# Performance work log

Measured on AMD Instinct MI355X. Metric: run time of the kernel, lower is better.

Reference implementation:

```python
import jax, jax.numpy as jnp
import numpy as np

EPS = 0.01
EXPD_WEIGHT = 1.0
COMP_WEIGHT = 1.0
NUM_CLASSES = 32
M, D = 262144, 128


def setup_inputs() -> dict:
    key = jax.random.key(0)
    k1, k2 = jax.random.split(key)
    cls_score = jax.random.normal(k1, (M, D), dtype=jnp.float32)
    label = jax.random.randint(k2, (M,), 0, NUM_CLASSES)
    return {"cls_score": cls_score, "label": label}


def _logdet(X):
    sgn, ld = jnp.linalg.slogdet(X)
    return sgn * ld


def reference(cls_score, label):
    m, d = cls_score.shape
    m_f = jnp.asarray(m, cls_score.dtype)
    # expansion term: logdet(c * Z^T Z) / 2, c = d / (m * eps)
    c = d / (m_f * EPS)
    cov = cls_score.T @ cls_score  # [d, d]
    loss_expd = _logdet(c * cov) / 2.0

    # compression term: sum_j m_j/(2m) * logdet(c_j * Z_j^T Z_j)
    def per_class(j):
        mask = (label == j).astype(cls_score.dtype)  # [m]
        m_j = mask.sum()
        safe_mj = jnp.maximum(m_j, 1.0)
        c_j = d / (safe_mj * EPS)
        # Z_j^T Z_j == (mask * Z)^T Z, honoring the boolean subset without gather
        cov_j = (cls_score * mask[:, None]).T @ cls_score  # [d, d]
        ld_j = _logdet(c_j * cov_j)
        return jnp.where(m_j > 0, ld_j * m_j / (2.0 * m_f), 0.0)

    comps = jax.lax.map(per_class, jnp.arange(NUM_CLASSES))  # [J]
    loss_comp = comps.sum()

    # MCR2Loss.forward with return_all=False
    return loss_comp * COMP_WEIGHT - loss_expd * EXPD_WEIGHT
```

## Files before the change

### kernel.cpp

```cpp
#include <hip/hip_runtime.h>
#include <math.h>

#define D 128
#define NCLS 32
#define TSLOT 16
#define CHUNK 256

typedef float f32x16 __attribute__((ext_vector_type(16)));
typedef short bf16x8 __attribute__((ext_vector_type(8)));

__global__ void zero_k(int* hist) {
  int t = threadIdx.x;
  if (t < NCLS) hist[t] = 0;
}

__global__ __launch_bounds__(64) void hist_blk_k(const int* __restrict__ label, int M,
                                                 int NB, int* __restrict__ blkhist_t,
                                                 int* __restrict__ hist) {
  __shared__ int h[NCLS];
  const int lane = threadIdx.x;
  const int b = blockIdx.x;
  if (lane < NCLS) h[lane] = 0;
  __syncthreads();
  const int s0 = b * CHUNK;
#pragma unroll
  for (int it = 0; it < CHUNK / 64; ++it) {
    int i = s0 + it * 64 + lane;
    if (i < M) atomicAdd(&h[label[i]], 1);
  }
  __syncthreads();
  if (lane < NCLS) {
    blkhist_t[lane * NB + b] = h[lane];
    atomicAdd(&hist[lane], h[lane]);
  }
}

__global__ void prefix_k(const int* __restrict__ hist, int* __restrict__ cstart) {
  if (threadIdx.x == 0) {
    int run = 0;
    for (int j = 0; j < NCLS; ++j) { cstart[j] = run; run += hist[j]; }
    cstart[NCLS] = run;
  }
}

__global__ __launch_bounds__(64) void base_k(const int* __restrict__ blkhist_t,
                                             const int* __restrict__ cstart, int NB,
                                             int* __restrict__ base_t) {
  const int j = blockIdx.x;
  const int lane = threadIdx.x;
  const int K = (NB + 63) / 64;
  int vals[32];
  int run = 0;
  for (int k = 0; k < K; ++k) {
    int b = lane * K + k;
    int v = (b < NB) ? blkhist_t[j * NB + b] : 0;
    vals[k] = v;
    run += v;
  }
  int incl = run;
  for (int off = 1; off < 64; off <<= 1) {
    int o = __shfl_up(incl, off);
    if (lane >= off) incl += o;
  }
  int pos = cstart[j] + (incl - run);
  for (int k = 0; k < K; ++k) {
    int b = lane * K + k;
    if (b < NB) base_t[j * NB + b] = pos;
    pos += vals[k];
  }
}

__global__ __launch_bounds__(64) void scatter2_k(const int* __restrict__ label, int M,
                                                 int NB, const int* __restrict__ base_t,
                                                 int* __restrict__ idxbuf) {
  __shared__ int cur[NCLS];
  const int b = blockIdx.x;
  const int lane = threadIdx.x;
  if (lane < NCLS) cur[lane] = base_t[lane * NB + b];
  __syncthreads();
  const int s0 = b * CHUNK;
#pragma unroll
  for (int it = 0; it < CHUNK / 64; ++it) {
    int i = s0 + it * 64 + lane;
    int j = (i < M) ? label[i] : -1;
    unsigned long long mask = 0;
#pragma unroll
    for (int q = 0; q < NCLS; ++q) {
      unsigned long long mm = __ballot(j == q);
      if (j == q) mask = mm;
    }
    if (j >= 0) {
      int myoff = __popcll(mask & ((1ull << lane) - 1ull));
      int basec = cur[j];
      idxbuf[basec + myoff] = i;
      if (myoff == 0) cur[j] = basec + __popcll(mask);
    }
    __syncthreads();
  }
}

__device__ inline void bsplit(float x, short& hi, short& lo) {
  unsigned u = __float_as_uint(x);
  unsigned rh = u + 0x7fffu + ((u >> 16) & 1u);
  unsigned short h = (unsigned short)(rh >> 16);
  float hf = __uint_as_float((unsigned)h << 16);
  float l = x - hf;
  unsigned ul = __float_as_uint(l);
  unsigned rl = ul + 0x7fffu + ((ul >> 16) & 1u);
  hi = (short)h;
  lo = (short)(rl >> 16);
}

__global__ __launch_bounds__(512, 4) void cov_k(const float* __restrict__ Z,
                                                const int* __restrict__ idxbuf,
                                                const int* __restrict__ hist,
                                                const int* __restrict__ cstart,
                                                float* __restrict__ partials) {
  __shared__ __attribute__((aligned(16))) char arena[66048];

  const int b = blockIdx.x;
  const int cls = b / TSLOT, slot = b % TSLOT;
  const int t = threadIdx.x;
  const int lane = t & 63;
  const int w = t >> 6;
  const int r = w & 3;
  const int pass = w >> 2;
  const int col4 = t & 31;
  const int rg = t >> 5;

  const int mj = hist[cls];
  const int seg0 = cstart[cls];
  const int segend = seg0 + mj;
  const int nch = (mj + 63) / 64;

  f32x16 acc[4];
#pragma unroll
  for (int c = 0; c < 4; ++c)
#pragma unroll
    for (int i = 0; i < 16; ++i) acc[c][i] = 0.f;

  const int pcol = r * 32 + (lane & 31);
  const int h = lane >> 5;
  const int aswz = (pcol & 7) << 4;
  char* const bbase = arena + (pass ? 16384 : 0);

  float4 pv[4];
  {
    const int ch = slot;
    const int r0 = seg0 + ch * 64;
#pragma unroll
    for (int i = 0; i < 4; ++i) {
      int gr = r0 + rg * 4 + i;
      if (ch < nch && gr < segend) {
        int ridx = idxbuf[gr];
        pv[i] = *(const float4*)(Z + (size_t)ridx * D + col4 * 4);
      } else {
        pv[i] = make_float4(0.f, 0.f, 0.f, 0.f);
      }
    }
  }

  for (int ch = slot; ch < nch; ch += TSLOT) {
    __syncthreads();
    {
      float xs[4][4];
      xs[0][0] = pv[0].x; xs[0][1] = pv[0].y; xs[0][2] = pv[0].z; xs[0][3] = pv[0].w;
      xs[1][0] = pv[1].x; xs[1][1] = pv[1].y; xs[1][2] = pv[1].z; xs[1][3] = pv[1].w;
      xs[2][0] = pv[2].x; xs[2][1] = pv[2].y; xs[2][2] = pv[2].z; xs[2][3] = pv[2].w;
      xs[3][0] = pv[3].x; xs[3][1] = pv[3].y; xs[3][2] = pv[3].z; xs[3][3] = pv[3].w;
#pragma unroll
      for (int j = 0; j < 4; ++j) {
        short h0, h1, h2, h3, l0, l1, l2, l3;
        bsplit(xs[0][j], h0, l0);
        bsplit(xs[1][j], h1, l1);
        bsplit(xs[2][j], h2, l2);
        bsplit(xs[3][j], h3, l3);
        const int cc = col4 * 4 + j;
        const int off = cc * 128 + ((rg * 8) ^ ((cc & 7) << 4));
        *(short4*)(arena + off) = make_short4(h0, h1, h2, h3);
        *(short4*)(arena + 16384 + off) = make_short4(l0, l1, l2, l3);
      }
    }
    __syncthreads();
    {
      const int chn = ch + TSLOT;
      const int r0 = seg0 + chn * 64;
#pragma unroll
      for (int i = 0; i < 4; ++i) {
        int gr = r0 + rg * 4 + i;
        if (chn < nch && gr < segend) {
          int ridx = idxbuf[gr];
          pv[i] = *(const float4*)(Z + (size_t)ridx * D + col4 * 4);
        } else {
          pv[i] = make_float4(0.f, 0.f, 0.f, 0.f);
        }
      }
    }
#pragma unroll
    for (int kk = 0; kk < 4; ++kk) {
      const int koff = kk * 32 + h * 16;
      bf16x8 a = *(const bf16x8*)(arena + pcol * 128 + (koff ^ aswz));
#pragma unroll
      for (int c = 0; c < 4; ++c) {
        const int qcol = c * 32 + (lane & 31);
        bf16x8 bb = *(const bf16x8*)(bbase + qcol * 128 + (koff ^ ((qcol & 7) << 4)));
        acc[c] = __builtin_amdgcn_mfma_f32_32x32x16_bf16(a, bb, acc[c], 0, 0, 0);
      }
    }
  }

  __syncthreads();
  float* g2 = (float*)arena;
  if (pass == 1) {
#pragma unroll
    for (int c = 0; c < 4; ++c)
#pragma unroll
      for (int i = 0; i < 16; ++i) {
        int prow = r * 32 + (i & 3) + 8 * (i >> 2) + 4 * h;
        int qcol = c * 32 + (lane & 31);
        g2[prow * 129 + qcol] = acc[c][i];
      }
  }
  __syncthreads();
  if (pass == 0) {
    size_t base = (size_t)b * (D * D);
#pragma unroll
    for (int c = 0; c < 4; ++c)
#pragma unroll
      for (int i = 0; i < 16; ++i) {
        int prow = r * 32 + (i & 3) + 8 * (i >> 2) + 4 * h;
        int qcol = c * 32 + (lane & 31);
        float v = acc[c][i] + g2[prow * 129 + qcol] + g2[qcol * 129 + prow];
        partials[base + (size_t)prow * D + qcol] = v;
      }
  }
}

__global__ void reduce_k(const float* __restrict__ partials, float* __restrict__ covs) {
  int e = blockIdx.x * blockDim.x + threadIdx.x;
  double tot = 0.0;
  for (int j = 0; j < NCLS; ++j) {
    double s = 0.0;
    for (int t = 0; t < TSLOT; ++t)
      s += (double)partials[(size_t)(j * TSLOT + t) * (D * D) + e];
    covs[(size_t)j * (D * D) + e] = (float)s;
    tot += s;
  }
  covs[(size_t)NCLS * (D * D) + e] = (float)tot;
}

template <int T>
__device__ void trailing_upd(float (*As)[132], int pbase, int tid) {
  const int ty = tid >> 4, tx = tid & 15;
  const int r0 = pbase + 32 + ty * T;
  const int c0 = pbase + 32 + tx * T;
  float acc[T][T];
#pragma unroll
  for (int a = 0; a < T; ++a)
#pragma unroll
    for (int b = 0; b < T; ++b) acc[a][b] = 0.f;
#pragma unroll
  for (int j0 = 0; j0 < 32; j0 += 8) {
    float ar[T][8];
#pragma unroll
    for (int a = 0; a < T; ++a) {
      float4 v0 = *(const float4*)&As[r0 + a][pbase + j0];
      float4 v1 = *(const float4*)&As[r0 + a][pbase + j0 + 4];
      ar[a][0] = v0.x; ar[a][1] = v0.y; ar[a][2] = v0.z; ar[a][3] = v0.w;
      ar[a][4] = v1.x; ar[a][5] = v1.y; ar[a][6] = v1.z; ar[a][7] = v1.w;
    }
#pragma unroll
    for (int b = 0; b < T; ++b) {
      float4 w0 = *(const float4*)&As[c0 + b][pbase + j0];
      float4 w1 = *(const float4*)&As[c0 + b][pbase + j0 + 4];
      float acb[8] = {w0.x, w0.y, w0.z, w0.w, w1.x, w1.y, w1.z, w1.w};
#pragma unroll
      for (int jj = 0; jj < 8; ++jj)
#pragma unroll
        for (int a = 0; a < T; ++a)
          acc[a][b] = fmaf(ar[a][jj], acb[jj], acc[a][b]);
    }
  }
#pragma unroll
  for (int a = 0; a < T; ++a)
#pragma unroll
    for (int b = 0; b < T; ++b)
      As[r0 + a][c0 + b] -= acc[a][b];
}

__global__ __launch_bounds__(256, 1) void chol_k(const float* __restrict__ covs,
                                                 const int* __restrict__ hist,
                                                 int Mtot, double* __restrict__ results) {
  __shared__ float As[128][132];
  __shared__ float PlT[32][36];
  __shared__ float invd[32];
  __shared__ float colbuf[32];
  __shared__ double red[64];
  const int j = blockIdx.x;
  const float* A = covs + (size_t)j * (D * D);
  const int tid = threadIdx.x;
  const int lane = tid & 63;
  const int w = tid >> 6;

#pragma unroll
  for (int it = 0; it < 16; ++it) {
    int e = it * 1024 + tid * 4;
    int r = e >> 7, c = e & 127;
    *(float4*)&As[r][c] = *(const float4*)&A[e];
  }
  __syncthreads();

  double lda = 0.0;
#pragma unroll 1
  for (int p = 0; p < 4; ++p) {
    const int pbase = p * 32;
    if (w == 0) {
      const int l = lane & 31;
      float row[32];
#pragma unroll
      for (int c4 = 0; c4 < 8; ++c4) {
        float4 v = *(const float4*)&As[pbase + l][pbase + c4 * 4];
        row[c4 * 4 + 0] = v.x; row[c4 * 4 + 1] = v.y;
        row[c4 * 4 + 2] = v.z; row[c4 * 4 + 3] = v.w;
      }
      float mypiv = 1.f, myinv = 0.f;
#pragma unroll
      for (int k = 0; k < 32; ++k) {
        colbuf[l] = row[k];
        float cb[32];
#pragma unroll
        for (int q = 0; q < 8; ++q) {
          float4 v = *(const float4*)&colbuf[q * 4];
          cb[q * 4 + 0] = v.x; cb[q * 4 + 1] = v.y;
          cb[q * 4 + 2] = v.z; cb[q * 4 + 3] = v.w;
        }
        float piv = cb[k];
        float inv = rsqrtf(piv);
        inv = inv * (1.5f - 0.5f * piv * inv * inv);
        if (lane == k) { mypiv = piv; myinv = inv; }
        float tmul = row[k] * (inv * inv);
#pragma unroll
        for (int c = k + 1; c < 32; ++c)
          row[c] = fmaf(-tmul, cb[c], row[c]);
        row[k] *= inv;
      }
      if (lane < 32) {
#pragma unroll
        for (int c = 0; c < 32; ++c) PlT[c][lane] = row[c];
        invd[lane] = myinv;
      }
      lda += log((double)mypiv);
    }
    __syncthreads();
    const int N2 = 96 - pbase;
    if (tid < N2) {
      const int R = pbase + 32 + tid;
      float s[32];
#pragma unroll
      for (int c4 = 0; c4 < 8; ++c4) {
        float4 v = *(const float4*)&As[R][pbase + c4 * 4];
        s[c4 * 4 + 0] = v.x; s[c4 * 4 + 1] = v.y;
        s[c4 * 4 + 2] = v.z; s[c4 * 4 + 3] = v.w;
      }
#pragma unroll
      for (int i = 0; i < 32; ++i) {
        float xi = s[i] * invd[i];
        s[i] = xi;
#pragma unroll
        for (int jj = i + 1; jj < 32; ++jj)
          s[jj] = fmaf(-xi, PlT[i][jj], s[jj]);
      }
#pragma unroll
      for (int c4 = 0; c4 < 8; ++c4)
        *(float4*)&As[R][pbase + c4 * 4] =
            make_float4(s[c4 * 4], s[c4 * 4 + 1], s[c4 * 4 + 2], s[c4 * 4 + 3]);
    }
    __syncthreads();
    if (N2 == 96) trailing_upd<6>(As, pbase, tid);
    else if (N2 == 64) trailing_upd<4>(As, pbase, tid);
    else if (N2 == 32) trailing_upd<2>(As, pbase, tid);
    __syncthreads();
  }

  if (w == 0) red[lane] = lda;
  __syncthreads();
  if (tid == 0) {
    double lsum = 0.0;
    for (int i = 0; i < 64; ++i) lsum += red[i];
    if (j < NCLS) {
      int mj = hist[j];
      double res = 0.0;
      if (mj > 0) {
        double cj = (double)D / ((double)mj * 0.01);
        res = ((double)D * log(cj) + lsum) * (double)mj / (2.0 * (double)Mtot);
      }
      results[j] = res;
    } else {
      double c = (double)D / ((double)Mtot * 0.01);
      results[NCLS] = ((double)D * log(c) + lsum) * 0.5;
    }
  }
}

__global__ void final_k(const double* __restrict__ results, float* __restrict__ out) {
  if (threadIdx.x == 0 && blockIdx.x == 0) {
    double s = 0.0;
    for (int j = 0; j < NCLS; ++j) s += results[j];
    out[0] = (float)(s - results[NCLS]);
  }
}

extern "C" void kernel_launch(void* const* d_in, const int* in_sizes, int n_in,
                              void* d_out, int out_size, void* d_ws, size_t ws_size,
                              hipStream_t stream) {
  const float* Z = (const float*)d_in[0];
  const int* label = (const int*)d_in[1];
  const int Mtot = in_sizes[1];
  float* out = (float*)d_out;
  const int NB = (Mtot + CHUNK - 1) / CHUNK;

  char* ws = (char*)d_ws;
  int* hist = (int*)(ws + 0);
  int* cstart = (int*)(ws + 256);
  double* results = (double*)(ws + 512);
  int* idxbuf = (int*)(ws + 1024);
  float* partials = (float*)(ws + 1024 + (size_t)Mtot * sizeof(int));
  float* covs = partials + (size_t)NCLS * TSLOT * D * D;
  int* blkhist_t = (int*)partials;
  int* base_t = blkhist_t + (size_t)NCLS * NB;

  zero_k<<<1, 64, 0, stream>>>(hist);
  hist_blk_k<<<NB, 64, 0, stream>>>(label, Mtot, NB, blkhist_t, hist);
  prefix_k<<<1, 64, 0, stream>>>(hist, cstart);
  base_k<<<NCLS, 64, 0, stream>>>(blkhist_t, cstart, NB, base_t);
  scatter2_k<<<NB, 64, 0, stream>>>(label, Mtot, NB, base_t, idxbuf);
  cov_k<<<NCLS * TSLOT, 512, 0, stream>>>(Z, idxbuf, hist, cstart, partials);
  reduce_k<<<(D * D) / 256, 256, 0, stream>>>(partials, covs);
  chol_k<<<NCLS + 1, 256, 0, stream>>>(covs, hist, Mtot, results);
  final_k<<<1, 64, 0, stream>>>(results, out);
}
```

Measured before the change: 129.8 us.

## Use split-bf16 MFMA for Cholesky trailing update in chol_k

Replaces the scalar FP32 trailing-submatrix SYRK update in the blocked Cholesky with MFMA 32x32x16 bf16 instructions. Each value is split into hi and lo bf16 parts, and three products (hi*hi, hi*lo, lo*hi) approximate FP32 accuracy. The solved panel is staged into new LDS buffers instead of being written back into As. The change only touches the small 128x128 factorization kernel, so its effect on total time is limited. It also risks losing precision in the logdet and leaving the L panel unstored, which is harmless only because just the diagonal is used.

```diff
diff --git a/kernel.cpp b/kernel.cpp
--- a/kernel.cpp
+++ b/kernel.cpp
@@ -249,45 +249,6 @@
   covs[(size_t)NCLS * (D * D) + e] = (float)tot;
 }
 
-template <int T>
-__device__ void trailing_upd(float (*As)[132], int pbase, int tid) {
-  const int ty = tid >> 4, tx = tid & 15;
-  const int r0 = pbase + 32 + ty * T;
-  const int c0 = pbase + 32 + tx * T;
-  float acc[T][T];
-#pragma unroll
-  for (int a = 0; a < T; ++a)
-#pragma unroll
-    for (int b = 0; b < T; ++b) acc[a][b] = 0.f;
-#pragma unroll
-  for (int j0 = 0; j0 < 32; j0 += 8) {
-    float ar[T][8];
-#pragma unroll
-    for (int a = 0; a < T; ++a) {
-      float4 v0 = *(const float4*)&As[r0 + a][pbase + j0];
-      float4 v1 = *(const float4*)&As[r0 + a][pbase + j0 + 4];
-      ar[a][0] = v0.x; ar[a][1] = v0.y; ar[a][2] = v0.z; ar[a][3] = v0.w;
-      ar[a][4] = v1.x; ar[a][5] = v1.y; ar[a][6] = v1.z; ar[a][7] = v1.w;
-    }
-#pragma unroll
-    for (int b = 0; b < T; ++b) {
-      float4 w0 = *(const float4*)&As[c0 + b][pbase + j0];
-      float4 w1 = *(const float4*)&As[c0 + b][pbase + j0 + 4];
-      float acb[8] = {w0.x, w0.y, w0.z, w0.w, w1.x, w1.y, w1.z, w1.w};
-#pragma unroll
-      for (int jj = 0; jj < 8; ++jj)
-#pragma unroll
-        for (int a = 0; a < T; ++a)
-          acc[a][b] = fmaf(ar[a][jj], acb[jj], acc[a][b]);
-    }
-  }
-#pragma unroll
-  for (int a = 0; a < T; ++a)
-#pragma unroll
-    for (int b = 0; b < T; ++b)
-      As[r0 + a][c0 + b] -= acc[a][b];
-}
-
 __global__ __launch_bounds__(256, 1) void chol_k(const float* __restrict__ covs,
                                                  const int* __restrict__ hist,
                                                  int Mtot, double* __restrict__ results) {
@@ -296,11 +257,13 @@
   __shared__ float invd[32];
   __shared__ float colbuf[32];
   __shared__ double red[64];
+  __shared__ __attribute__((aligned(16))) short Thi[96 * 40];
+  __shared__ __attribute__((aligned(16))) short Tlo[96 * 40];
   const int j = blockIdx.x;
   const float* A = covs + (size_t)j * (D * D);
   const int tid = threadIdx.x;
   const int lane = tid & 63;
-  const int w = tid >> 6;
+  const int wv = tid >> 6;
 
 #pragma unroll
   for (int it = 0; it < 16; ++it) {
@@ -314,7 +277,8 @@
 #pragma unroll 1
   for (int p = 0; p < 4; ++p) {
     const int pbase = p * 32;
-    if (w == 0) {
+    const int N2 = 96 - pbase;
+    if (wv == 0) {
       const int l = lane & 31;
       float row[32];
 #pragma unroll
@@ -352,7 +316,6 @@
       lda += log((double)mypiv);
     }
     __syncthreads();
-    const int N2 = 96 - pbase;
     if (tid < N2) {
       const int R = pbase + 32 + tid;
       float s[32];
@@ -370,19 +333,58 @@
         for (int jj = i + 1; jj < 32; ++jj)
           s[jj] = fmaf(-xi, PlT[i][jj], s[jj]);
       }
-#pragma unroll
-      for (int c4 = 0; c4 < 8; ++c4)
-        *(float4*)&As[R][pbase + c4 * 4] =
-            make_float4(s[c4 * 4], s[c4 * 4 + 1], s[c4 * 4 + 2], s[c4 * 4 + 3]);
-    }
-    __syncthreads();
-    if (N2 == 96) trailing_upd<6>(As, pbase, tid);
-    else if (N2 == 64) trailing_upd<4>(As, pbase, tid);
-    else if (N2 == 32) trailing_upd<2>(As, pbase, tid);
-    __syncthreads();
-  }
-
-  if (w == 0) red[lane] = lda;
+      unsigned hp[16], lp[16];
+#pragma unroll
+      for (int q = 0; q < 16; ++q) {
+        short ha, la, hb, lb;
+        bsplit(s[2 * q], ha, la);
+        bsplit(s[2 * q + 1], hb, lb);
+        hp[q] = (unsigned)(unsigned short)ha | ((unsigned)(unsigned short)hb << 16);
+        lp[q] = (unsigned)(unsigned short)la | ((unsigned)(unsigned short)lb << 16);
+      }
+#pragma unroll
+      for (int q = 0; q < 4; ++q) {
+        *(int4*)&Thi[tid * 40 + q * 8] =
+            make_int4(hp[4 * q], hp[4 * q + 1], hp[4 * q + 2], hp[4 * q + 3]);
+        *(int4*)&Tlo[tid * 40 + q * 8] =
+            make_int4(lp[4 * q], lp[4 * q + 1], lp[4 * q + 2], lp[4 * q + 3]);
+      }
+    }
+    __syncthreads();
+    const int nstr = N2 >> 5;
+    if (wv < nstr) {
+      const int l31 = lane & 31;
+      const int h = lane >> 5;
+      const int arow = wv * 32 + l31;
+#pragma unroll 1
+      for (int ct = 0; ct < nstr; ++ct) {
+        const int brow = ct * 32 + l31;
+        f32x16 acc;
+#pragma unroll
+        for (int i = 0; i < 16; ++i) acc[i] = 0.f;
+#pragma unroll
+        for (int ks = 0; ks < 2; ++ks) {
+          const int off = ks * 16 + h * 8;
+          bf16x8 ahi = *(const bf16x8*)&Thi[arow * 40 + off];
+          bf16x8 alo = *(const bf16x8*)&Tlo[arow * 40 + off];
+          bf16x8 bhi = *(const bf16x8*)&Thi[brow * 40 + off];
+          bf16x8 blo = *(const bf16x8*)&Tlo[brow * 40 + off];
+          acc = __builtin_amdgcn_mfma_f32_32x32x16_bf16(ahi, bhi, acc, 0, 0, 0);
+          acc = __builtin_amdgcn_mfma_f32_32x32x16_bf16(ahi, blo, acc, 0, 0, 0);
+          acc = __builtin_amdgcn_mfma_f32_32x32x16_bf16(alo, bhi, acc, 0, 0, 0);
+        }
+#pragma unroll
+        for (int i = 0; i < 16; ++i) {
+          int rr = pbase + 32 + wv * 32 + (i & 3) + 8 * (i >> 2) + 4 * h;
+          int cc = pbase + 32 + ct * 32 + l31;
+          As[rr][cc] -= acc[i];
+        }
+      }
+    }
+    __syncthreads();
+  }
+
+  if (wv == 0) red[lane] = lda;
   __syncthreads();
   if (tid == 0) {
     double lsum = 0.0;
```

After: 126.3 us. 2.6% less time.
